# Performance work log

Measured on AMD Instinct MI355X. Metric: run time of the kernel, lower is better.

## Reference

```python
import jax, jax.numpy as jnp
import numpy as np
from jax import lax

C = 16        # class_nums
START = 14    # tag_to_idx['<START>']
STOP = 15     # tag_to_idx['<STOP>']
NEG = -10000.0
B, T, V, E, H = 64, 512, 50000, 512, 1024
HD = H // 2   # per-direction hidden size


def setup_inputs() -> dict:
    key = jax.random.key(0)
    ks = jax.random.split(key, 16)
    s = 0.05
    inp = {}
    inp["sentence"] = jax.random.randint(ks[0], (B, T), 0, V)
    inp["embedding"] = jax.random.normal(ks[1], (V, E), jnp.float32) * 0.1
    # LSTM params, torch layout: [4*HD, Din] with gate order i,f,g,o; leading dim 2 = (fwd, bwd)
    inp["w_ih_l0"] = jax.random.normal(ks[2], (2, 4 * HD, E), jnp.float32) * s
    inp["w_hh_l0"] = jax.random.normal(ks[3], (2, 4 * HD, HD), jnp.float32) * s
    inp["b_ih_l0"] = jax.random.normal(ks[4], (2, 4 * HD), jnp.float32) * s
    inp["b_hh_l0"] = jax.random.normal(ks[5], (2, 4 * HD), jnp.float32) * s
    inp["w_ih_l1"] = jax.random.normal(ks[6], (2, 4 * HD, H), jnp.float32) * s
    inp["w_hh_l1"] = jax.random.normal(ks[7], (2, 4 * HD, HD), jnp.float32) * s
    inp["b_ih_l1"] = jax.random.normal(ks[8], (2, 4 * HD), jnp.float32) * s
    inp["b_hh_l1"] = jax.random.normal(ks[9], (2, 4 * HD), jnp.float32) * s
    inp["lin_w"] = jax.random.normal(ks[10], (C, H), jnp.float32) * s
    inp["lin_b"] = jax.random.normal(ks[11], (C,), jnp.float32) * s
    tr = jax.random.normal(ks[12], (C, C), jnp.float32)
    inp["transitions"] = tr.at[START, :].set(NEG).at[:, STOP].set(NEG)
    # init_hidden(): random (h0, c0), shape [2*num_layers, B, HD]
    inp["h0"] = jax.random.normal(ks[13], (4, B, HD), jnp.float32)
    inp["c0"] = jax.random.normal(ks[14], (4, B, HD), jnp.float32)
    return inp


def _lstm_dir(x, w_ih, w_hh, b_ih, b_hh, h0, c0, reverse):
    # x: [T, B, Din] -> hs: [T, B, HD]
    def step(carry, xt):
        h, c = carry
        g = xt @ w_ih.T + h @ w_hh.T + b_ih + b_hh  # [B, 4*HD]
        i, f, gc, o = jnp.split(g, 4, axis=-1)       # torch gate order: i, f, g, o
        c = jax.nn.sigmoid(f) * c + jax.nn.sigmoid(i) * jnp.tanh(gc)
        h = jax.nn.sigmoid(o) * jnp.tanh(c)
        return (h, c), h
    _, hs = lax.scan(step, (h0, c0), x, reverse=reverse)
    return hs


def _features(sentence, embedding, w_ih_l0, w_hh_l0, b_ih_l0, b_hh_l0,
              w_ih_l1, w_hh_l1, b_ih_l1, b_hh_l1, lin_w, lin_b, h0, c0):
    x = embedding[sentence].transpose(1, 0, 2)  # [T, B, E]
    # layer 0 (bidirectional)
    hf = _lstm_dir(x, w_ih_l0[0], w_hh_l0[0], b_ih_l0[0], b_hh_l0[0], h0[0], c0[0], False)
    hb = _lstm_dir(x, w_ih_l0[1], w_hh_l0[1], b_ih_l0[1], b_hh_l0[1], h0[1], c0[1], True)
    x = jnp.concatenate([hf, hb], axis=-1)      # [T, B, H]
    # layer 1 (bidirectional)
    hf = _lstm_dir(x, w_ih_l1[0], w_hh_l1[0], b_ih_l1[0], b_hh_l1[0], h0[2], c0[2], False)
    hb = _lstm_dir(x, w_ih_l1[1], w_hh_l1[1], b_ih_l1[1], b_hh_l1[1], h0[3], c0[3], True)
    x = jnp.concatenate([hf, hb], axis=-1)      # [T, B, H]
    feats = x @ lin_w.T + lin_b                 # [T, B, C]
    return feats.transpose(1, 0, 2)             # [B, T, C]


def _viterbi(feats, transitions):
    # feats: [T, C]. Vectorized over the tag dim; scan over time.
    init = jnp.full((C,), NEG, feats.dtype).at[START].set(0.0)

    def step(fv, feat_t):
        scores = fv[None, :] + transitions      # [next_tag, prev_tag]
        bp = jnp.argmax(scores, axis=1)
        return jnp.max(scores, axis=1) + feat_t, bp

    fv, bps = lax.scan(step, init, feats)       # bps: [T, C]
    terminal = fv + transitions[STOP]
    best = jnp.argmax(terminal)

    def back(tag, bp_t):
        return bp_t[tag], tag

    _, path = lax.scan(back, best, bps, reverse=True)  # [T]
    return terminal[best], path


def reference(sentence, embedding, w_ih_l0, w_hh_l0, b_ih_l0, b_hh_l0,
              w_ih_l1, w_hh_l1, b_ih_l1, b_hh_l1, lin_w, lin_b,
              transitions, h0, c0):
    feats = _features(sentence, embedding, w_ih_l0, w_hh_l0, b_ih_l0, b_hh_l0,
                      w_ih_l1, w_hh_l1, b_ih_l1, b_hh_l1, lin_w, lin_b, h0, c0)
    scores, paths = jax.vmap(_viterbi, in_axes=(0, None))(feats, transitions)
    return scores, paths
```

## Files before the change

### kernel.cpp

```cpp
#include <hip/hip_runtime.h>
#include <stdint.h>

constexpr int kB  = 64;
constexpr int kT  = 512;
constexpr int kHD = 512;
constexpr int kC  = 16;
constexpr int kL  = 32;
constexpr int kSTART = 14;
constexpr int kSTOP  = 15;
#define NEGV (-10000.0f)

typedef __bf16 bf16x8 __attribute__((ext_vector_type(8)));
typedef float  f32x4  __attribute__((ext_vector_type(4)));

union U16x8 { uint4 u; bf16x8 v; };

__device__ __forceinline__ unsigned short f2bf(float f) {
    union { float f; unsigned int u; } x; x.f = f;
    unsigned int u = x.u;
    u += 0x7fffu + ((u >> 16) & 1u);
    return (unsigned short)(u >> 16);
}
__device__ __forceinline__ float bf2f(unsigned int hbits) {
    union { unsigned int u; float f; } x; x.u = hbits << 16;
    return x.f;
}
__device__ __forceinline__ float fsig(float x) {
    return __builtin_amdgcn_rcpf(1.f + __expf(-x));
}
__device__ __forceinline__ float ftanh(float x) {
    float e = __expf(2.f * x);
    return 1.f - 2.f * __builtin_amdgcn_rcpf(e + 1.f);
}

typedef __attribute__((address_space(1))) const unsigned int GASU;
typedef __attribute__((address_space(3))) unsigned int LASU;
__device__ __forceinline__ void ld_lds16(const unsigned short* g, unsigned short* l) {
    __builtin_amdgcn_global_load_lds((GASU*)g, (LASU*)l, 16, 0, 0);
}


__global__ void k_castWx(const float* __restrict__ src, unsigned short* __restrict__ dst, int K) {
    int np = blockIdx.x;
    int dd = np >> 11, r = np & 2047;
    int g = r & 3, cj = r >> 2;
    const float* s = src + ((size_t)(dd * 2048 + g * 512 + cj)) * K;
    unsigned short* d = dst + (size_t)np * K;
    for (int e = threadIdx.x * 8; e < K; e += 128 * 8) {
        float4 a = *(const float4*)(s + e);
        float4 b = *(const float4*)(s + e + 4);
        ushort4 lo, hi;
        lo.x = f2bf(a.x); lo.y = f2bf(a.y); lo.z = f2bf(a.z); lo.w = f2bf(a.w);
        hi.x = f2bf(b.x); hi.y = f2bf(b.y); hi.z = f2bf(b.z); hi.w = f2bf(b.w);
        *(ushort4*)(d + e) = lo; *(ushort4*)(d + e + 4) = hi;
    }
}

__global__ void k_embed(const int* __restrict__ sent, const float* __restrict__ emb,
                        unsigned short* __restrict__ X0) {
    int row = blockIdx.x;
    int t = row >> 6, b = row & 63;
    int v = sent[b * kT + t];
    const float4* src = (const float4*)(emb + (size_t)v * 512);
    float4 f = src[threadIdx.x];
    ushort4 o;
    o.x = f2bf(f.x); o.y = f2bf(f.y); o.z = f2bf(f.z); o.w = f2bf(f.w);
    ((ushort4*)(X0 + (size_t)row * 512))[threadIdx.x] = o;
}

__global__ void k_init(const float* __restrict__ h0, const float* __restrict__ c0,
                       const float* __restrict__ bih0, const float* __restrict__ bhh0,
                       const float* __restrict__ bih1, const float* __restrict__ bhh1,
                       const float* __restrict__ lw,
                       unsigned long long* __restrict__ Xex, float* __restrict__ ccur,
                       float* __restrict__ biascat0, float* __restrict__ biascat1,
                       unsigned short* __restrict__ lwb) {
    int i = blockIdx.x * blockDim.x + threadIdx.x;
    const int NS = 4 * kB * kHD;
    const int NX = 65536;
    if (i < NS) {
        ccur[i] = c0[i];
    } else if (i < NS + 8192) {
        int j2 = i - NS;
        int l = j2 >> 12;
        int n = j2 & 4095;
        int dd = n >> 11, r = n & 2047;
        int g = r >> 9, cj = r & 511;
        float v = l ? (bih1[n] + bhh1[n]) : (bih0[n] + bhh0[n]);
        int np = dd * 2048 + cj * 4 + g;
        (l ? biascat1 : biascat0)[np] = v;
    } else if (i < NS + 8192 + 16384) {
        int idx = i - NS - 8192;
        lwb[idx] = f2bf(lw[idx]);
    } else if (i < NS + 8192 + 16384 + NX) {
        int u = i - (NS + 8192 + 16384);
        int l = u >> 15, rem = u & 32767;
        int d = rem >> 14, rem2 = rem & 16383;
        int b = rem2 >> 8, q2 = rem2 & 255;
        int j0 = q2 * 2;
        const float* hp = h0 + ((size_t)(l * 2 + d) * 64 + b) * 512 + j0;
        unsigned int pay = (unsigned)f2bf(hp[0]) | ((unsigned)f2bf(hp[1]) << 16);
        Xex[(size_t)l * 65536 + ((size_t)d * 64 + b) * 256 + q2] = (unsigned long long)pay;
    } else if (i < NS + 8192 + 16384 + 2 * NX) {
        int u = i - (NS + 8192 + 16384 + NX);
        int l = u >> 15, rem = u & 32767;
        Xex[(size_t)l * 65536 + 32768 + rem] = 0ull;
    }
}

__launch_bounds__(256, 2)
__global__ void k_gemm(const unsigned short* __restrict__ A,
                       const unsigned short* __restrict__ Bm,
                       const float* __restrict__ bias,
                       unsigned short* __restrict__ Cm,
                       int K, int afwd, int abwd) {
    const int nb = blockIdx.x & 31;
    const int mb = blockIdx.x >> 5;
    const int m0w = mb << 7;
    const int arow0 = (m0w < 2048) ? (afwd + m0w) : (abwd + (m0w - 2048));
    const int n0 = nb << 7;
    const int tid = threadIdx.x;
    const int lane = tid & 63;
    const int wave = tid >> 6;
    const int wm = wave >> 1, wn = wave & 1;
    const int l16 = lane & 15, quad = lane >> 4;
    __shared__ unsigned short As[128 * 32];
    __shared__ unsigned short Bs[128 * 32];
    const int srw = wave * 32 + (lane >> 2);
    const int sc  = lane & 3;
    unsigned short* AsW0 = As + wave * 1024;
    unsigned short* AsW1 = As + wave * 1024 + 512;
    unsigned short* BsW0 = Bs + wave * 1024;
    unsigned short* BsW1 = Bs + wave * 1024 + 512;

    f32x4 acc[4][4];
    #pragma unroll
    for (int i = 0; i < 4; ++i)
        #pragma unroll
        for (int jj = 0; jj < 4; ++jj) acc[i][jj] = (f32x4){0,0,0,0};

    const int kiters = K >> 5;
    for (int kk = 0; kk < kiters; ++kk) {
        __syncthreads();
        ld_lds16(A  + (size_t)(arow0 + srw)      * K + kk * 32 + sc * 8, AsW0);
        ld_lds16(A  + (size_t)(arow0 + srw + 16) * K + kk * 32 + sc * 8, AsW1);
        ld_lds16(Bm + (size_t)(n0 + srw)         * K + kk * 32 + sc * 8, BsW0);
        ld_lds16(Bm + (size_t)(n0 + srw + 16)    * K + kk * 32 + sc * 8, BsW1);
        __syncthreads();
        U16x8 af[4], bf[4];
        #pragma unroll
        for (int i = 0; i < 4; ++i) {
            af[i].u = *(const uint4*)(As + (wm * 64 + i * 16 + l16) * 32 + quad * 8);
            bf[i].u = *(const uint4*)(Bs + (wn * 64 + i * 16 + l16) * 32 + quad * 8);
        }
        #pragma unroll
        for (int i = 0; i < 4; ++i)
            #pragma unroll
            for (int jj = 0; jj < 4; ++jj)
                acc[i][jj] = __builtin_amdgcn_mfma_f32_16x16x32_bf16(af[i].v, bf[jj].v, acc[i][jj], 0, 0, 0);
    }
    #pragma unroll
    for (int jj = 0; jj < 4; ++jj) {
        int n = n0 + wn * 64 + jj * 16 + l16;
        float bv = bias[n];
        #pragma unroll
        for (int i = 0; i < 4; ++i) {
            int mrow = m0w + wm * 64 + i * 16 + quad * 4;
            #pragma unroll
            for (int rr = 0; rr < 4; ++rr)
                Cm[(size_t)(mrow + rr) * 4096 + n] = f2bf(acc[i][jj][rr] + bv);
        }
    }
}

__launch_bounds__(512, 1)
__global__ void k_fused(const unsigned short* __restrict__ Wh,
                        const unsigned short* __restrict__ Gx,
                        unsigned long long* __restrict__ Xex,
                        float* __restrict__ cc,
                        unsigned short* __restrict__ hs,
                        unsigned short* __restrict__ S,
                        int s0, int split,
                        const unsigned short* __restrict__ Ag,
                        const unsigned short* __restrict__ Wxg,
                        const float* __restrict__ biasg,
                        unsigned short* __restrict__ Gxout,
                        int Kg, int gfwd, int gbwd, int do_gemm) {
    __shared__ __align__(16) char smem[52928];
    const int tid = threadIdx.x;

    if (blockIdx.x < 64) {
        unsigned short* zbuf   = (unsigned short*)smem;
        float*          gsAll  = (float*)(smem + 33280);
        unsigned short* hstU16 = (unsigned short*)(smem + 50688);
        unsigned long long* hU = (unsigned long long*)(smem + 50688);
        const int blk = blockIdx.x;
        const int d  = blk >> 5;
        const int bh = (blk >> 4) & 1;
        const int wc = blk & 15;
        const int wave = tid >> 6;
        const int lane = tid & 63;
        const int l16 = lane & 15;
        const int quad = lane >> 4;
        const int r4 = lane >> 2;
        const int u  = lane & 3;
        const int col = wc * 32 + wave * 4 + u;
        float* gw = gsAll + wave * 544;
        const int r8 = tid >> 3, u8 = tid & 7;

        uint4 wreg[16];
        {
            const unsigned short* wrow =
                Wh + ((size_t)d * 2048 + wc * 128 + wave * 16 + l16) * 512 + quad * 8;
            #pragma unroll
            for (int kk = 0; kk < 16; ++kk) wreg[kk] = *(const uint4*)(wrow + kk * 32);
        }
        float cst[2];
        #pragma unroll
        for (int mt = 0; mt < 2; ++mt)
            cst[mt] = cc[((size_t)d * 64 + bh * 32 + mt * 16 + r4) * 512 + col];

        for (int sl = 0; sl < kL; ++sl) {
            const int s = s0 + sl;
            const int t = d ? (kT - 1 - s) : s;
            ushort4 gx4[2];
            #pragma unroll
            for (int mt = 0; mt < 2; ++mt) {
                int b = bh * 32 + mt * 16 + r4;
                int grow = d ? (2048 + (kL - 1 - sl) * 64 + b) : (sl * 64 + b);
                gx4[mt] = *(const ushort4*)(Gx + (size_t)grow * 4096 + d * 2048 + col * 4);
            }
            {
                const unsigned long long* xb =
                    Xex + ((size_t)((s & 1) * 2 + d) * 64 + bh * 32) * 256;
                const unsigned sq = (unsigned)s;
                unsigned long long va[8], vb[8];
                #pragma unroll
                for (int k = 0; k < 8; ++k) {
                    int idx = tid + k * 512;
                    int r = idx >> 7, q = idx & 127;
                    const unsigned long long* p = xb + r * 256 + q * 2;
                    va[k] = __hip_atomic_load(p,     __ATOMIC_RELAXED, __HIP_MEMORY_SCOPE_AGENT);
                    vb[k] = __hip_atomic_load(p + 1, __ATOMIC_RELAXED, __HIP_MEMORY_SCOPE_AGENT);
                }
                for (;;) {
                    int stale = 0;
                    #pragma unroll
                    for (int k = 0; k < 8; ++k) {
                        int idx = tid + k * 512;
                        int r = idx >> 7, q = idx & 127;
                        const unsigned long long* p = xb + r * 256 + q * 2;
                        if ((unsigned)(va[k] >> 32) < sq) {
                            va[k] = __hip_atomic_load(p, __ATOMIC_RELAXED, __HIP_MEMORY_SCOPE_AGENT);
                            stale = 1;
                        }
                        if ((unsigned)(vb[k] >> 32) < sq) {
                            vb[k] = __hip_atomic_load(p + 1, __ATOMIC_RELAXED, __HIP_MEMORY_SCOPE_AGENT);
                            stale = 1;
                        }
                    }
                    if (!stale) break;
                }
                #pragma unroll
                for (int k = 0; k < 8; ++k) {
                    int idx = tid + k * 512;
                    int r = idx >> 7, q = idx & 127;
                    unsigned long long pay = (va[k] & 0xffffffffull) | (vb[k] << 32);
                    *(unsigned long long*)(zbuf + r * 520 + q * 4) = pay;
                }
            }
            __syncthreads();
            f32x4 acc[2];
            acc[0] = (f32x4){0, 0, 0, 0};
            acc[1] = (f32x4){0, 0, 0, 0};
            #pragma unroll
            for (int kk = 0; kk < 16; ++kk) {
                U16x8 b; b.u = wreg[kk];
                #pragma unroll
                for (int mt = 0; mt < 2; ++mt) {
                    U16x8 a; a.u = *(const uint4*)(zbuf + (mt * 16 + l16) * 520 + kk * 32 + quad * 8);
                    acc[mt] = __builtin_amdgcn_mfma_f32_16x16x32_bf16(a.v, b.v, acc[mt], 0, 0, 0);
                }
            }
            #pragma unroll
            for (int mt = 0; mt < 2; ++mt)
                #pragma unroll
                for (int rr = 0; rr < 4; ++rr)
                    gw[mt * 272 + (quad * 4 + rr) * 17 + l16] = acc[mt][rr];
            asm volatile("s_waitcnt lgkmcnt(0)" ::: "memory");
            __builtin_amdgcn_sched_barrier(0);
            #pragma unroll
            for (int mt = 0; mt < 2; ++mt) {
                const float* gb = gw + mt * 272 + r4 * 17 + u * 4;
                float gi = gb[0] + bf2f(gx4[mt].x);
                float gf = gb[1] + bf2f(gx4[mt].y);
                float gg = gb[2] + bf2f(gx4[mt].z);
                float go = gb[3] + bf2f(gx4[mt].w);
                float si = fsig(gi);
                float sf = fsig(gf);
                float so = fsig(go);
                float tg = ftanh(gg);
                float cn = sf * cst[mt] + si * tg;
                cst[mt] = cn;
                float hn = so * ftanh(cn);
                hstU16[(wave * 35 + mt * 16 + r4) * 4 + u] = f2bf(hn);
            }
            __syncthreads();
            if (tid < 256) {
                unsigned long long hv = hU[u8 * 35 + r8];
                unsigned long long sq1 = (unsigned long long)(unsigned)(s + 1) << 32;
                unsigned long long A  = (hv & 0xffffffffull) | sq1;
                unsigned long long Bv = (hv >> 32) | sq1;
                unsigned long long* xw =
                    Xex + ((size_t)(((s + 1) & 1) * 2 + d) * 64 + bh * 32 + r8) * 256
                        + (wc * 8 + u8) * 2;
                __hip_atomic_store(xw,     A,  __ATOMIC_RELAXED, __HIP_MEMORY_SCOPE_AGENT);
                __hip_atomic_store(xw + 1, Bv, __ATOMIC_RELAXED, __HIP_MEMORY_SCOPE_AGENT);
            } else {
                int q = tid - 256;
                int r = q >> 3, uu = q & 7;
                unsigned long long val = hU[uu * 35 + r];
                int b = bh * 32 + r;
                bool toS = split && (d ? (t >= 256) : (t < 256));
                if (toS)
                    *(unsigned long long*)(S + ((size_t)t * 64 + b) * 512 + wc * 32 + uu * 4) = val;
                else
                    *(unsigned long long*)(hs + ((size_t)t * 64 + b) * 1024 + (size_t)d * 512 + wc * 32 + uu * 4) = val;
            }
        }
        #pragma unroll
        for (int mt = 0; mt < 2; ++mt)
            cc[((size_t)d * 64 + bh * 32 + mt * 16 + r4) * 512 + col] = cst[mt];
    } else {
        if (!do_gemm) return;
        const int gw = blockIdx.x - 64;
        const int half = tid >> 8;
        const int tid2 = tid & 255;
        const int w4 = tid2 >> 6;
        const int lane = tid2 & 63;
        const int l16 = lane & 15, quad = lane >> 4;
        unsigned short* As = (unsigned short*)(smem + half * 16384);
        unsigned short* Bs = (unsigned short*)(smem + half * 16384 + 8192);
        const int srw = w4 * 32 + (lane >> 2);
        const int sc  = lane & 3;
        const int wm = w4 >> 1, wn = w4 & 1;
        unsigned short* AsW0 = As + w4 * 1024;
        unsigned short* AsW1 = As + w4 * 1024 + 512;
        unsigned short* BsW0 = Bs + w4 * 1024;
        unsigned short* BsW1 = Bs + w4 * 1024 + 512;
        const int kiters = Kg >> 5;

        for (int pp = gw; pp < 512; pp += 192) {
            const int mb = pp >> 4;
            const int nb = ((pp & 15) << 1) + half;
            const int m0w = mb << 7;
            const int arow0 = (m0w < 2048) ? (gfwd + m0w) : (gbwd + (m0w - 2048));
            const int n0 = nb << 7;
            f32x4 acc[4][4];
            #pragma unroll
            for (int i = 0; i < 4; ++i)
                #pragma unroll
                for (int jj = 0; jj < 4; ++jj) acc[i][jj] = (f32x4){0,0,0,0};
            for (int kk = 0; kk < kiters; ++kk) {
                __syncthreads();
                ld_lds16(Ag  + (size_t)(arow0 + srw)      * Kg + kk * 32 + sc * 8, AsW0);
                ld_lds16(Ag  + (size_t)(arow0 + srw + 16) * Kg + kk * 32 + sc * 8, AsW1);
                ld_lds16(Wxg + (size_t)(n0 + srw)         * Kg + kk * 32 + sc * 8, BsW0);
                ld_lds16(Wxg + (size_t)(n0 + srw + 16)    * Kg + kk * 32 + sc * 8, BsW1);
                __syncthreads();
                U16x8 af[4], bf[4];
                #pragma unroll
                for (int i = 0; i < 4; ++i) {
                    af[i].u = *(const uint4*)(As + (wm * 64 + i * 16 + l16) * 32 + quad * 8);
                    bf[i].u = *(const uint4*)(Bs + (wn * 64 + i * 16 + l16) * 32 + quad * 8);
                }
                #pragma unroll
                for (int i = 0; i < 4; ++i)
                    #pragma unroll
                    for (int jj = 0; jj < 4; ++jj)
                        acc[i][jj] = __builtin_amdgcn_mfma_f32_16x16x32_bf16(af[i].v, bf[jj].v, acc[i][jj], 0, 0, 0);
            }
            #pragma unroll
            for (int jj = 0; jj < 4; ++jj) {
                int n = n0 + wn * 64 + jj * 16 + l16;
                float bv = biasg[n];
                #pragma unroll
                for (int i = 0; i < 4; ++i) {
                    int mrow = m0w + wm * 64 + i * 16 + quad * 4;
                    #pragma unroll
                    for (int rr = 0; rr < 4; ++rr)
                        Gxout[(size_t)(mrow + rr) * 4096 + n] = f2bf(acc[i][jj][rr] + bv);
                }
            }
        }
    }
}

__global__ void k_linear(const unsigned short* __restrict__ hs1,
                         const unsigned short* __restrict__ S,
                         const unsigned short* __restrict__ lwb,
                         const float* __restrict__ lb,
                         float* __restrict__ feats) {
    const int t = blockIdx.x;
    const int tid = threadIdx.x;
    const int wave = tid >> 6;
    const int lane = tid & 63;
    const int l16 = lane & 15, quad = lane >> 4;
    __shared__ unsigned short lws[16 * 1032];
    {
        #pragma unroll
        for (int i = 0; i < 8; ++i) {
            int idx = tid + i * 256;
            int n = idx >> 7, c = idx & 127;
            *(uint4*)(lws + n * 1032 + c * 8) = *(const uint4*)(lwb + n * 1024 + c * 8);
        }
    }
    __syncthreads();
    const int brow = wave * 16 + l16;
    f32x4 acc = {0, 0, 0, 0};
    #pragma unroll
    for (int kk = 0; kk < 32; ++kk) {
        int k0 = kk * 32 + quad * 8;
        const unsigned short* p;
        if (kk < 16)
            p = (t < 256) ? S   + ((size_t)t * 64 + brow) * 512  + k0
                          : hs1 + ((size_t)t * 64 + brow) * 1024 + k0;
        else
            p = (t >= 256) ? S   + ((size_t)t * 64 + brow) * 512  + (k0 - 512)
                           : hs1 + ((size_t)t * 64 + brow) * 1024 + k0;
        U16x8 a; a.u = *(const uint4*)p;
        U16x8 b; b.u = *(const uint4*)(lws + l16 * 1032 + k0);
        acc = __builtin_amdgcn_mfma_f32_16x16x32_bf16(a.v, b.v, acc, 0, 0, 0);
    }
    float bv = lb[l16];
    #pragma unroll
    for (int rr = 0; rr < 4; ++rr) {
        int b = wave * 16 + quad * 4 + rr;
        feats[(size_t)b * (kT * kC) + t * kC + l16] = acc[rr] + bv;
    }
}

__global__ void k_viterbi(const float* __restrict__ feats, const float* __restrict__ trans,
                          float* __restrict__ out) {
    int b = blockIdx.x;
    int lane = threadIdx.x;
    __shared__ unsigned char bp[kT * kC];
    __shared__ float fv[2][kC];
    __shared__ float tbuf[kC];
    float trow[16];
    float tstop = 0.f;
    if (lane < 16) {
        #pragma unroll
        for (int p = 0; p < 16; ++p) trow[p] = trans[lane * 16 + p];
        tstop = trans[kSTOP * 16 + lane];
        fv[0][lane] = (lane == kSTART) ? 0.f : NEGV;
    }
    __syncthreads();
    const float* fb = feats + (size_t)b * (kT * kC);
    for (int t = 0; t < kT; ++t) {
        if (lane < 16) {
            float m = -3.4e38f; int arg = 0;
            #pragma unroll
            for (int p = 0; p < 16; ++p) {
                float v = fv[t & 1][p] + trow[p];
                if (v > m) { m = v; arg = p; }
            }
            bp[t * 16 + lane] = (unsigned char)arg;
            fv[(t + 1) & 1][lane] = m + fb[t * 16 + lane];
        }
        __syncthreads();
    }
    if (lane < 16) tbuf[lane] = fv[kT & 1][lane] + tstop;
    __syncthreads();
    if (lane == 0) {
        float bm = tbuf[0]; int best = 0;
        #pragma unroll
        for (int p = 1; p < 16; ++p) if (tbuf[p] > bm) { bm = tbuf[p]; best = p; }
        out[b] = bm;
        float* path = out + kB + (size_t)b * kT;
        int tag = best;
        for (int t = kT - 1; t >= 0; --t) {
            path[t] = (float)tag;
            tag = bp[t * 16 + tag];
        }
    }
}

extern "C" void kernel_launch(void* const* d_in, const int* in_sizes, int n_in,
                              void* d_out, int out_size, void* d_ws, size_t ws_size,
                              hipStream_t stream) {
    const int*   sent = (const int*)d_in[0];
    const float* emb  = (const float*)d_in[1];
    const float* wih0 = (const float*)d_in[2];
    const float* whh0 = (const float*)d_in[3];
    const float* bih0 = (const float*)d_in[4];
    const float* bhh0 = (const float*)d_in[5];
    const float* wih1 = (const float*)d_in[6];
    const float* whh1 = (const float*)d_in[7];
    const float* bih1 = (const float*)d_in[8];
    const float* bhh1 = (const float*)d_in[9];
    const float* lw   = (const float*)d_in[10];
    const float* lb   = (const float*)d_in[11];
    const float* tr   = (const float*)d_in[12];
    const float* h0   = (const float*)d_in[13];
    const float* c0   = (const float*)d_in[14];
    float* out = (float*)d_out;

    char* ws = (char*)d_ws;
    size_t off = 0;
    auto alloc = [&](size_t bytes) -> void* {
        void* p = ws + off; off += (bytes + 255) & ~(size_t)255; return p;
    };
    unsigned short* X0    = (unsigned short*)alloc((size_t)kT * kB * 512 * 2);
    unsigned short* Wx0   = (unsigned short*)alloc((size_t)4096 * 512 * 2);
    unsigned short* S     = (unsigned short*)X0;
    unsigned short* Wh0   = (unsigned short*)alloc((size_t)4096 * 512 * 2);
    unsigned short* Wx1   = (unsigned short*)alloc((size_t)4096 * 1024 * 2);
    unsigned short* Wh1   = (unsigned short*)alloc((size_t)4096 * 512 * 2);
    float*          biascat0 = (float*)alloc(4096 * 4);
    float*          biascat1 = (float*)alloc(4096 * 4);
    unsigned short* HS    = (unsigned short*)alloc((size_t)kT * kB * 1024 * 2);
    unsigned long long* Xex = (unsigned long long*)alloc((size_t)2 * 65536 * 8);
    float*          ccur  = (float*)alloc((size_t)4 * kB * kHD * 4);
    float*          feats = (float*)alloc((size_t)kB * kT * kC * 4);
    unsigned short* lwb   = (unsigned short*)alloc(16384 * 2);
    unsigned short* Gx0   = (unsigned short*)alloc((size_t)4096 * 4096 * 2);
    unsigned short* Gx1   = (unsigned short*)alloc((size_t)4096 * 4096 * 2);
    unsigned short* GxB[2] = {Gx0, Gx1};

    k_castWx<<<4096, 128, 0, stream>>>(wih0, Wx0, 512);
    k_castWx<<<4096, 128, 0, stream>>>(whh0, Wh0, 512);
    k_castWx<<<4096, 128, 0, stream>>>(wih1, Wx1, 1024);
    k_castWx<<<4096, 128, 0, stream>>>(whh1, Wh1, 512);
    k_init<<<(131072 + 8192 + 16384 + 2 * 65536) / 256, 256, 0, stream>>>(
        h0, c0, bih0, bhh0, bih1, bhh1, lw, Xex, ccur, biascat0, biascat1, lwb);
    k_embed<<<kT * kB, 128, 0, stream>>>(sent, emb, X0);

    unsigned long long* Xex1 = Xex + (size_t)65536;
    float*              ccur1 = ccur + (size_t)65536;

    k_gemm<<<1024, 256, 0, stream>>>(X0, Wx0, biascat0, Gx0, 512, 0, (kT - kL) * 64);
    for (int ch = 0; ch < 16; ++ch) {
        int s0n = (ch + 1) * kL;
        k_fused<<<256, 512, 0, stream>>>(Wh0, GxB[ch & 1], Xex, ccur, HS, S, ch * kL, 0,
                                         X0, Wx0, biascat0, GxB[(ch + 1) & 1], 512,
                                         s0n * 64, (kT - kL - s0n) * 64, ch < 15);
    }
    k_gemm<<<1024, 256, 0, stream>>>(HS, Wx1, biascat1, Gx0, 1024, 0, (kT - kL) * 64);
    for (int ch = 0; ch < 16; ++ch) {
        int s0n = (ch + 1) * kL;
        k_fused<<<256, 512, 0, stream>>>(Wh1, GxB[ch & 1], Xex1, ccur1, HS, S, ch * kL, 1,
                                         HS, Wx1, biascat1, GxB[(ch + 1) & 1], 1024,
                                         s0n * 64, (kT - kL - s0n) * 64, ch < 15);
    }

    k_linear<<<kT, 256, 0, stream>>>(HS, S, lwb, lb, feats);
    k_viterbi<<<kB, 64, 0, stream>>>(feats, tr, out);
}
```

Measured before the change: 4.673 ms.

## Share A tile across GEMM halves, add spin backoff, shuffle-based Viterbi

New measurement: 4.759 ms. About the same (+1.8%).

```diff
diff --git a/kernel.cpp b/kernel.cpp
--- a/kernel.cpp
+++ b/kernel.cpp
@@ -260,6 +260,7 @@
                         }
                     }
                     if (!stale) break;
+                    __builtin_amdgcn_s_sleep(1);
                 }
                 #pragma unroll
                 for (int k = 0; k < 8; ++k) {
@@ -339,23 +340,21 @@
         const int w4 = tid2 >> 6;
         const int lane = tid2 & 63;
         const int l16 = lane & 15, quad = lane >> 4;
-        unsigned short* As = (unsigned short*)(smem + half * 16384);
-        unsigned short* Bs = (unsigned short*)(smem + half * 16384 + 8192);
-        const int srw = w4 * 32 + (lane >> 2);
-        const int sc  = lane & 3;
+        unsigned short* As  = (unsigned short*)smem;
+        unsigned short* Bs0 = As + 4096;
+        unsigned short* Bs1 = As + 8192;
+        unsigned short* Bsh = half ? Bs1 : Bs0;
         const int wm = w4 >> 1, wn = w4 & 1;
-        unsigned short* AsW0 = As + w4 * 1024;
-        unsigned short* AsW1 = As + w4 * 1024 + 512;
-        unsigned short* BsW0 = Bs + w4 * 1024;
-        unsigned short* BsW1 = Bs + w4 * 1024 + 512;
+        const int sr = tid >> 2;
+        const int sc = tid & 3;
         const int kiters = Kg >> 5;
 
         for (int pp = gw; pp < 512; pp += 192) {
             const int mb = pp >> 4;
-            const int nb = ((pp & 15) << 1) + half;
+            const int nb0 = (pp & 15) << 1;
             const int m0w = mb << 7;
             const int arow0 = (m0w < 2048) ? (gfwd + m0w) : (gbwd + (m0w - 2048));
-            const int n0 = nb << 7;
+            const int n00 = nb0 << 7;
             f32x4 acc[4][4];
             #pragma unroll
             for (int i = 0; i < 4; ++i)
@@ -363,16 +362,15 @@
                 for (int jj = 0; jj < 4; ++jj) acc[i][jj] = (f32x4){0,0,0,0};
             for (int kk = 0; kk < kiters; ++kk) {
                 __syncthreads();
-                ld_lds16(Ag  + (size_t)(arow0 + srw)      * Kg + kk * 32 + sc * 8, AsW0);
-                ld_lds16(Ag  + (size_t)(arow0 + srw + 16) * Kg + kk * 32 + sc * 8, AsW1);
-                ld_lds16(Wxg + (size_t)(n0 + srw)         * Kg + kk * 32 + sc * 8, BsW0);
-                ld_lds16(Wxg + (size_t)(n0 + srw + 16)    * Kg + kk * 32 + sc * 8, BsW1);
+                ld_lds16(Ag  + (size_t)(arow0 + sr)       * Kg + kk * 32 + sc * 8, As  + tid * 8);
+                ld_lds16(Wxg + (size_t)(n00 + sr)         * Kg + kk * 32 + sc * 8, Bs0 + tid * 8);
+                ld_lds16(Wxg + (size_t)(n00 + 128 + sr)   * Kg + kk * 32 + sc * 8, Bs1 + tid * 8);
                 __syncthreads();
                 U16x8 af[4], bf[4];
                 #pragma unroll
                 for (int i = 0; i < 4; ++i) {
-                    af[i].u = *(const uint4*)(As + (wm * 64 + i * 16 + l16) * 32 + quad * 8);
-                    bf[i].u = *(const uint4*)(Bs + (wn * 64 + i * 16 + l16) * 32 + quad * 8);
+                    af[i].u = *(const uint4*)(As  + (wm * 64 + i * 16 + l16) * 32 + quad * 8);
+                    bf[i].u = *(const uint4*)(Bsh + (wn * 64 + i * 16 + l16) * 32 + quad * 8);
                 }
                 #pragma unroll
                 for (int i = 0; i < 4; ++i)
@@ -380,6 +378,7 @@
                     for (int jj = 0; jj < 4; ++jj)
                         acc[i][jj] = __builtin_amdgcn_mfma_f32_16x16x32_bf16(af[i].v, bf[jj].v, acc[i][jj], 0, 0, 0);
             }
+            const int n0 = (nb0 + half) << 7;
             #pragma unroll
             for (int jj = 0; jj < 4; ++jj) {
                 int n = n0 + wn * 64 + jj * 16 + l16;
@@ -445,37 +444,50 @@
     int b = blockIdx.x;
     int lane = threadIdx.x;
     __shared__ unsigned char bp[kT * kC];
-    __shared__ float fv[2][kC];
-    __shared__ float tbuf[kC];
     float trow[16];
     float tstop = 0.f;
+    float fv = NEGV;
     if (lane < 16) {
         #pragma unroll
         for (int p = 0; p < 16; ++p) trow[p] = trans[lane * 16 + p];
         tstop = trans[kSTOP * 16 + lane];
-        fv[0][lane] = (lane == kSTART) ? 0.f : NEGV;
-    }
-    __syncthreads();
+        fv = (lane == kSTART) ? 0.f : NEGV;
+    }
     const float* fb = feats + (size_t)b * (kT * kC);
-    for (int t = 0; t < kT; ++t) {
-        if (lane < 16) {
+    float f0 = (lane < 16) ? fb[lane] : 0.f;
+    float f1 = (lane < 16) ? fb[16 + lane] : 0.f;
+    for (int t = 0; t < kT; t += 2) {
+        float f2 = (lane < 16 && t + 2 < kT) ? fb[(t + 2) * 16 + lane] : 0.f;
+        float f3 = (lane < 16 && t + 3 < kT) ? fb[(t + 3) * 16 + lane] : 0.f;
+        {
             float m = -3.4e38f; int arg = 0;
             #pragma unroll
             for (int p = 0; p < 16; ++p) {
-                float v = fv[t & 1][p] + trow[p];
+                float v = __shfl(fv, p, 16) + trow[p];
                 if (v > m) { m = v; arg = p; }
             }
-            bp[t * 16 + lane] = (unsigned char)arg;
-            fv[(t + 1) & 1][lane] = m + fb[t * 16 + lane];
-        }
-        __syncthreads();
-    }
-    if (lane < 16) tbuf[lane] = fv[kT & 1][lane] + tstop;
+            if (lane < 16) { bp[t * 16 + lane] = (unsigned char)arg; fv = m + f0; }
+        }
+        {
+            float m = -3.4e38f; int arg = 0;
+            #pragma unroll
+            for (int p = 0; p < 16; ++p) {
+                float v = __shfl(fv, p, 16) + trow[p];
+                if (v > m) { m = v; arg = p; }
+            }
+            if (lane < 16) { bp[(t + 1) * 16 + lane] = (unsigned char)arg; fv = m + f1; }
+        }
+        f0 = f2; f1 = f3;
+    }
+    float term = fv + tstop;
+    float bm = -3.4e38f; int best = 0;
+    #pragma unroll
+    for (int p = 0; p < 16; ++p) {
+        float v = __shfl(term, p, 16);
+        if (v > bm) { bm = v; best = p; }
+    }
     __syncthreads();
     if (lane == 0) {
-        float bm = tbuf[0]; int best = 0;
-        #pragma unroll
-        for (int p = 1; p < 16; ++p) if (tbuf[p] > bm) { bm = tbuf[p]; best = p; }
         out[b] = bm;
         float* path = out + kB + (size_t)b * kT;
         int tag = best;
```
